# Optimization experiments

Hardware: AMD Instinct MI355X
Metric: run time of the kernel (lower is better)

The kernel has to match this reference:

```python
import jax, jax.numpy as jnp
import numpy as np

N_IN, N_OUT, H = 32, 31, 128
B1, B2 = 256, 256


def setup_inputs() -> dict:
    key = jax.random.key(0)
    ks = jax.random.split(key, 6)
    def lin(k, o, i):
        return jax.random.normal(k, (o, i), jnp.float32) / np.float32(np.sqrt(i))
    return {
        "t": jax.random.uniform(ks[0], (), jnp.float32),
        "y": jax.random.normal(ks[1], (B1, B2, N_OUT), jnp.float32),
        "W0": lin(ks[2], H, N_IN), "b0": jnp.zeros((H,), jnp.float32),
        "W1": lin(ks[3], H, H),    "b1": jnp.zeros((H,), jnp.float32),
        "W2": lin(ks[4], H, H),    "b2": jnp.zeros((H,), jnp.float32),
        "W3": lin(ks[5], N_OUT, H), "b3": jnp.zeros((N_OUT,), jnp.float32),
    }


def reference(t, y, W0, b0, W1, b1, W2, b2, W3, b3):
    # inp[..., :-1] = y ; inp[..., -1] = force(t) with force = sin
    force = jnp.sin(t)
    inp = jnp.concatenate(
        [y, jnp.broadcast_to(force, y.shape[:-1] + (1,))], axis=-1
    )  # [B1, B2, N_IN]

    def model(x):  # x: [N_IN]
        h = jnp.tanh(W0 @ x + b0)
        h = jnp.tanh(W1 @ h + b1)
        h = jnp.tanh(W2 @ h + b2)
        return W3 @ h + b3  # [N_OUT]

    out = jax.vmap(jax.vmap(model))(inp)  # [B1, B2, N_OUT]
    # vmap(vmap(jacrev(model)))(inp)[..., :-1] -> drop d/d(force) column
    jac = jax.vmap(jax.vmap(jax.jacrev(model)))(inp)[..., :-1]  # [B1,B2,N_OUT,N_IN-1]
    return out, jac
```

## Files before the change

kernel.cpp:

```cpp
#include <hip/hip_runtime.h>
#include <hip/hip_bf16.h>
#include <math.h>


using short8 = __attribute__((ext_vector_type(8))) short;
using f32x4  = __attribute__((ext_vector_type(4))) float;

#define WAVES 8
#define PB 4
#define PPB 32
#define STRIDE 136

__device__ __forceinline__ float fast_tanh(float z) {
    float e = __expf(2.0f * z);
    return 1.0f - 2.0f * __builtin_amdgcn_rcpf(e + 1.0f);
}

__device__ __forceinline__ ushort f2bf(float f) {
    union { float f; unsigned u; } v; v.f = f;
    unsigned r = v.u + 0x7fffu + ((v.u >> 16) & 1u);
    return (ushort)(r >> 16);
}

__device__ __forceinline__ short8 pack8(const float* s) {
    union { ushort u[8]; short8 v; } r;
    #pragma unroll
    for (int i = 0; i < 8; ++i) r.u[i] = f2bf(s[i]);
    return r.v;
}

__global__ void __launch_bounds__(512, 4)
node_mfma(const float* __restrict__ tptr,
          const float* __restrict__ y,
          const float* __restrict__ W0, const float* __restrict__ b0,
          const float* __restrict__ W1, const float* __restrict__ b1,
          const float* __restrict__ W2, const float* __restrict__ b2,
          const float* __restrict__ W3, const float* __restrict__ b3,
          float* __restrict__ out, float* __restrict__ jac, int npts) {
    __shared__ ushort XT[PB][32][STRIDE];
    __shared__ float  xb[PB][32];

    const int tid  = threadIdx.x;
    const int w    = tid >> 6;
    const int lane = tid & 63;
    const int r16  = lane & 15;
    const int g    = lane >> 4;
    const int j    = 16 * w + r16;

    float w0f[8];
    {
        const float4* p4 = reinterpret_cast<const float4*>(W0 + j * 32 + g * 8);
        float4 q0 = p4[0], q1 = p4[1];
        w0f[0]=q0.x; w0f[1]=q0.y; w0f[2]=q0.z; w0f[3]=q0.w;
        w0f[4]=q1.x; w0f[5]=q1.y; w0f[6]=q1.z; w0f[7]=q1.w;
    }
    short8 aW[2][4];
    #pragma unroll
    for (int L = 0; L < 2; ++L) {
        const float* WL = L ? W2 : W1;
        #pragma unroll
        for (int kc = 0; kc < 4; ++kc) {
            float tmp[8];
            const float4* p4 = reinterpret_cast<const float4*>(WL + j * 128 + kc * 32 + g * 8);
            float4 q0 = p4[0], q1 = p4[1];
            tmp[0]=q0.x; tmp[1]=q0.y; tmp[2]=q0.z; tmp[3]=q0.w;
            tmp[4]=q1.x; tmp[5]=q1.y; tmp[6]=q1.z; tmp[7]=q1.w;
            aW[L][kc] = pack8(tmp);
        }
    }
    const int mw = (w >> 1) & 1, nw = w & 1;
    const int r3 = 16 * mw + r16;
    short8 aW3[4];
    #pragma unroll
    for (int kc = 0; kc < 4; ++kc) {
        float tmp[8];
        if (r3 < 31) {
            const float4* p4 = reinterpret_cast<const float4*>(W3 + r3 * 128 + kc * 32 + g * 8);
            float4 q0 = p4[0], q1 = p4[1];
            tmp[0]=q0.x; tmp[1]=q0.y; tmp[2]=q0.z; tmp[3]=q0.w;
            tmp[4]=q1.x; tmp[5]=q1.y; tmp[6]=q1.z; tmp[7]=q1.w;
        } else {
            #pragma unroll
            for (int i = 0; i < 8; ++i) tmp[i] = 0.0f;
        }
        aW3[kc] = pack8(tmp);
    }
    const float b0v = b0[j];
    float bv[2][4], b3v[4];
    #pragma unroll
    for (int reg = 0; reg < 4; ++reg) {
        bv[0][reg] = b1[16 * w + 4 * g + reg];
        bv[1][reg] = b2[16 * w + 4 * g + reg];
        int o = 16 * mw + 4 * g + reg;
        b3v[reg] = (o < 31) ? b3[o] : 0.0f;
    }
    const float force = sinf(tptr[0]);

    for (int pass = 0; pass < PPB / PB; ++pass) {
        const int pbase = blockIdx.x * PPB + pass * PB;

        if (tid < PB * 32) {
            int pl = tid >> 5, c = tid & 31;
            float v = 0.0f;
            if (pbase + pl < npts) v = (c < 31) ? y[(size_t)(pbase + pl) * 31 + c] : force;
            xb[pl][c] = v;
        }
        __syncthreads();

        #pragma unroll
        for (int pl = 0; pl < PB; ++pl) {
            float zp = 0.0f;
            #pragma unroll
            for (int i = 0; i < 8; ++i) zp = fmaf(w0f[i], xb[pl][g * 8 + i], zp);
            zp += __shfl_xor(zp, 16, 64);
            zp += __shfl_xor(zp, 32, 64);
            float h = fast_tanh(zp + b0v);
            float d = 1.0f - h * h;
            #pragma unroll
            for (int i = 0; i < 8; ++i) {
                int c = g * 8 + i;
                XT[pl][c][j] = f2bf((c == 31) ? h : d * w0f[i]);
            }
        }
        __syncthreads();

        #pragma unroll
        for (int L = 0; L < 2; ++L) {
            uint2 stashA[PB], stashB[PB];
            #pragma unroll
            for (int pl = 0; pl < PB; ++pl) {
                f32x4 a0 = {0.f, 0.f, 0.f, 0.f}, a1 = {0.f, 0.f, 0.f, 0.f};
                #pragma unroll
                for (int kc = 0; kc < 4; ++kc) {
                    short8 bf0 = *reinterpret_cast<const short8*>(&XT[pl][r16][kc * 32 + g * 8]);
                    short8 bf1 = *reinterpret_cast<const short8*>(&XT[pl][16 + r16][kc * 32 + g * 8]);
                    a0 = __builtin_amdgcn_mfma_f32_16x16x32_bf16(aW[L][kc], bf0, a0, 0, 0, 0);
                    a1 = __builtin_amdgcn_mfma_f32_16x16x32_bf16(aW[L][kc], bf1, a1, 0, 0, 0);
                }
                union { ushort u[4]; uint2 v; } pa, pb;
                #pragma unroll
                for (int reg = 0; reg < 4; ++reg) {
                    float tv = fast_tanh(a1[reg] + bv[L][reg]);
                    float d  = 1.0f - tv * tv;
                    float dd = __shfl(d, lane | 15, 64);
                    pa.u[reg] = f2bf(dd * a0[reg]);
                    pb.u[reg] = (r16 == 15) ? f2bf(tv) : f2bf(dd * a1[reg]);
                }
                stashA[pl] = pa.v; stashB[pl] = pb.v;
            }
            __syncthreads();
            #pragma unroll
            for (int pl = 0; pl < PB; ++pl) {
                *reinterpret_cast<uint2*>(&XT[pl][r16][16 * w + 4 * g])      = stashA[pl];
                *reinterpret_cast<uint2*>(&XT[pl][16 + r16][16 * w + 4 * g]) = stashB[pl];
            }
            __syncthreads();
        }

        #pragma unroll
        for (int tsk = 0; tsk < 2; ++tsk) {
            int pl = (w >> 2) + tsk * 2;
            f32x4 a = {0.f, 0.f, 0.f, 0.f};
            #pragma unroll
            for (int kc = 0; kc < 4; ++kc) {
                short8 bf = *reinterpret_cast<const short8*>(&XT[pl][16 * nw + r16][kc * 32 + g * 8]);
                a = __builtin_amdgcn_mfma_f32_16x16x32_bf16(aW3[kc], bf, a, 0, 0, 0);
            }
            size_t p = (size_t)(pbase + pl);
            int c = 16 * nw + r16;
            if ((int)p < npts) {
                #pragma unroll
                for (int reg = 0; reg < 4; ++reg) {
                    int o = 16 * mw + 4 * g + reg;
                    if (o < 31) {
                        if (c == 31) out[p * 31 + o] = a[reg] + b3v[reg];
                        else         jac[(p * 31 + o) * 31 + c] = a[reg];
                    }
                }
            }
        }
        __syncthreads();
    }
}

extern "C" void kernel_launch(void* const* d_in, const int* in_sizes, int n_in,
                              void* d_out, int out_size, void* d_ws, size_t ws_size,
                              hipStream_t stream) {
    const float* t  = (const float*)d_in[0];
    const float* y  = (const float*)d_in[1];
    const float* W0 = (const float*)d_in[2];
    const float* b0 = (const float*)d_in[3];
    const float* W1 = (const float*)d_in[4];
    const float* b1 = (const float*)d_in[5];
    const float* W2 = (const float*)d_in[6];
    const float* b2 = (const float*)d_in[7];
    const float* W3 = (const float*)d_in[8];
    const float* b3 = (const float*)d_in[9];

    const int npts = in_sizes[1] / 31;
    float* out = (float*)d_out;
    float* jac = out + (size_t)npts * 31;

    const int blocks = (npts + PPB - 1) / PPB;
    node_mfma<<<blocks, 512, 0, stream>>>(t, y, W0, b0, W1, b1, W2, b2, W3, b3,
                                          out, jac, npts);
}
```

Baseline: 385.8 us.

## Stage Jacobian outputs in LDS for coalesced stores and use packed bf16 conversion

Jacobian and output tiles are first written into shared memory (reusing the XT buffer) and then stored to global memory with contiguous per-point writes. Before, each lane scattered strided stores straight from the MFMA accumulators. The layer-0 Jacobian seed is rebuilt from a bf16 transposed copy of W0 in LDS plus staged h/d vectors, and each thread writes packed 4-element chunks instead of 8 scalar bf16 stores. The f2bf bit trick is replaced by the hardware v_cvt_pk_bf16_f32 instruction. This adds extra barriers and LDS traffic, and the layer-0 seed now uses a bf16-rounded W0 rather than the fp32 W0.

Result: slower. 403.6 us (+4.6%).

```diff
diff --git a/kernel.cpp b/kernel.cpp
--- a/kernel.cpp
+++ b/kernel.cpp
@@ -6,7 +6,6 @@
 using short8 = __attribute__((ext_vector_type(8))) short;
 using f32x4  = __attribute__((ext_vector_type(4))) float;
 
-#define WAVES 8
 #define PB 4
 #define PPB 32
 #define STRIDE 136
@@ -16,16 +15,27 @@
     return 1.0f - 2.0f * __builtin_amdgcn_rcpf(e + 1.0f);
 }
 
-__device__ __forceinline__ ushort f2bf(float f) {
+__device__ __forceinline__ unsigned pk2(float lo, float hi) {
+    unsigned r;
+    asm("v_cvt_pk_bf16_f32 %0, %1, %2" : "=v"(r) : "v"(lo), "v"(hi));
+    return r;
+}
+
+__device__ __forceinline__ float bf2f(ushort u) {
+    union { unsigned u; float f; } c; c.u = ((unsigned)u) << 16;
+    return c.f;
+}
+
+__device__ __forceinline__ ushort f2bf1(float f) {
     union { float f; unsigned u; } v; v.f = f;
     unsigned r = v.u + 0x7fffu + ((v.u >> 16) & 1u);
     return (ushort)(r >> 16);
 }
 
-__device__ __forceinline__ short8 pack8(const float* s) {
-    union { ushort u[8]; short8 v; } r;
-    #pragma unroll
-    for (int i = 0; i < 8; ++i) r.u[i] = f2bf(s[i]);
+__device__ __forceinline__ short8 pack8f(const float* s) {
+    union { unsigned u[4]; short8 v; } r;
+    #pragma unroll
+    for (int q = 0; q < 4; ++q) r.u[q] = pk2(s[2 * q], s[2 * q + 1]);
     return r.v;
 }
 
@@ -37,8 +47,14 @@
           const float* __restrict__ W2, const float* __restrict__ b2,
           const float* __restrict__ W3, const float* __restrict__ b3,
           float* __restrict__ out, float* __restrict__ jac, int npts) {
-    __shared__ ushort XT[PB][32][STRIDE];
-    __shared__ float  xb[PB][32];
+    __shared__ __align__(16) ushort XT[PB][32][STRIDE];
+    __shared__ __align__(16) ushort W0T[32][128];
+    __shared__ __align__(16) float  d0s[PB][128];
+    __shared__ __align__(16) float  h0s[PB][128];
+    __shared__ float xb[PB][32];
+    __shared__ float ostage[PB][31];
+
+    float* jstage = reinterpret_cast<float*>(&XT[0][0][0]);
 
     const int tid  = threadIdx.x;
     const int w    = tid >> 6;
@@ -47,6 +63,11 @@
     const int g    = lane >> 4;
     const int j    = 16 * w + r16;
 
+    for (int e = tid; e < 4096; e += 512) {
+        int jj = e >> 5, c = e & 31;
+        W0T[c][jj] = f2bf1(W0[e]);
+    }
+
     float w0f[8];
     {
         const float4* p4 = reinterpret_cast<const float4*>(W0 + j * 32 + g * 8);
@@ -65,7 +86,7 @@
             float4 q0 = p4[0], q1 = p4[1];
             tmp[0]=q0.x; tmp[1]=q0.y; tmp[2]=q0.z; tmp[3]=q0.w;
             tmp[4]=q1.x; tmp[5]=q1.y; tmp[6]=q1.z; tmp[7]=q1.w;
-            aW[L][kc] = pack8(tmp);
+            aW[L][kc] = pack8f(tmp);
         }
     }
     const int mw = (w >> 1) & 1, nw = w & 1;
@@ -83,7 +104,7 @@
             #pragma unroll
             for (int i = 0; i < 8; ++i) tmp[i] = 0.0f;
         }
-        aW3[kc] = pack8(tmp);
+        aW3[kc] = pack8f(tmp);
     }
     const float b0v = b0[j];
     float bv[2][4], b3v[4];
@@ -115,12 +136,30 @@
             zp += __shfl_xor(zp, 16, 64);
             zp += __shfl_xor(zp, 32, 64);
             float h = fast_tanh(zp + b0v);
-            float d = 1.0f - h * h;
-            #pragma unroll
-            for (int i = 0; i < 8; ++i) {
-                int c = g * 8 + i;
-                XT[pl][c][j] = f2bf((c == 31) ? h : d * w0f[i]);
-            }
+            if (g == 0) {
+                h0s[pl][j] = h;
+                d0s[pl][j] = 1.0f - h * h;
+            }
+        }
+        __syncthreads();
+
+        #pragma unroll
+        for (int it = 0; it < 8; ++it) {
+            int idx = (it << 9) + tid;
+            int pl = idx >> 10, rem = idx & 1023;
+            int c = rem >> 5, jq = rem & 31;
+            float v0, v1, v2, v3;
+            if (c == 31) {
+                float4 hv = *reinterpret_cast<const float4*>(&h0s[pl][4 * jq]);
+                v0 = hv.x; v1 = hv.y; v2 = hv.z; v3 = hv.w;
+            } else {
+                float4 dv = *reinterpret_cast<const float4*>(&d0s[pl][4 * jq]);
+                ushort4 wv = *reinterpret_cast<const ushort4*>(&W0T[c][4 * jq]);
+                v0 = bf2f(wv.x) * dv.x; v1 = bf2f(wv.y) * dv.y;
+                v2 = bf2f(wv.z) * dv.z; v3 = bf2f(wv.w) * dv.w;
+            }
+            uint2 o; o.x = pk2(v0, v1); o.y = pk2(v2, v3);
+            *reinterpret_cast<uint2*>(&XT[pl][c][4 * jq]) = o;
         }
         __syncthreads();
 
@@ -137,16 +176,19 @@
                     a0 = __builtin_amdgcn_mfma_f32_16x16x32_bf16(aW[L][kc], bf0, a0, 0, 0, 0);
                     a1 = __builtin_amdgcn_mfma_f32_16x16x32_bf16(aW[L][kc], bf1, a1, 0, 0, 0);
                 }
-                union { ushort u[4]; uint2 v; } pa, pb;
+                float va[4], vb[4];
                 #pragma unroll
                 for (int reg = 0; reg < 4; ++reg) {
                     float tv = fast_tanh(a1[reg] + bv[L][reg]);
                     float d  = 1.0f - tv * tv;
                     float dd = __shfl(d, lane | 15, 64);
-                    pa.u[reg] = f2bf(dd * a0[reg]);
-                    pb.u[reg] = (r16 == 15) ? f2bf(tv) : f2bf(dd * a1[reg]);
+                    va[reg] = dd * a0[reg];
+                    vb[reg] = (r16 == 15) ? tv : dd * a1[reg];
                 }
-                stashA[pl] = pa.v; stashB[pl] = pb.v;
+                uint2 pa, pb;
+                pa.x = pk2(va[0], va[1]); pa.y = pk2(va[2], va[3]);
+                pb.x = pk2(vb[0], vb[1]); pb.y = pk2(vb[2], vb[3]);
+                stashA[pl] = pa; stashB[pl] = pb;
             }
             __syncthreads();
             #pragma unroll
@@ -157,6 +199,7 @@
             __syncthreads();
         }
 
+        f32x4 at[2];
         #pragma unroll
         for (int tsk = 0; tsk < 2; ++tsk) {
             int pl = (w >> 2) + tsk * 2;
@@ -166,18 +209,37 @@
                 short8 bf = *reinterpret_cast<const short8*>(&XT[pl][16 * nw + r16][kc * 32 + g * 8]);
                 a = __builtin_amdgcn_mfma_f32_16x16x32_bf16(aW3[kc], bf, a, 0, 0, 0);
             }
-            size_t p = (size_t)(pbase + pl);
+            at[tsk] = a;
+        }
+        __syncthreads();
+
+        #pragma unroll
+        for (int tsk = 0; tsk < 2; ++tsk) {
+            int pl = (w >> 2) + tsk * 2;
             int c = 16 * nw + r16;
+            #pragma unroll
+            for (int reg = 0; reg < 4; ++reg) {
+                int o = 16 * mw + 4 * g + reg;
+                if (o < 31) {
+                    if (c == 31)      ostage[pl][o] = at[tsk][reg] + b3v[reg];
+                    else              jstage[pl * 961 + o * 31 + c] = at[tsk][reg];
+                }
+            }
+        }
+        __syncthreads();
+
+        #pragma unroll
+        for (int pl = 0; pl < PB; ++pl) {
+            size_t p = (size_t)pbase + pl;
             if ((int)p < npts) {
-                #pragma unroll
-                for (int reg = 0; reg < 4; ++reg) {
-                    int o = 16 * mw + 4 * g + reg;
-                    if (o < 31) {
-                        if (c == 31) out[p * 31 + o] = a[reg] + b3v[reg];
-                        else         jac[(p * 31 + o) * 31 + c] = a[reg];
-                    }
-                }
-            }
+                for (int e = tid; e < 961; e += 512)
+                    jac[p * 961 + e] = jstage[pl * 961 + e];
+            }
+        }
+        if (tid < 128) {
+            int pl = tid >> 5, o = tid & 31;
+            if (o < 31 && pbase + pl < npts)
+                out[(size_t)(pbase + pl) * 31 + o] = ostage[pl][o];
         }
         __syncthreads();
     }
```

## Double-buffer activations in LDS, prefetch next y, use packed bf16 convert

Applied to the files above, without the earlier changes.

Splits the shared activation tile into two buffers so each hidden layer writes its output into the other buffer. This removes one barrier per layer and the register stash, and the barrier at the end of each pass is also dropped. The next pass's input row is prefetched from global memory into a register while the current pass computes. Float-to-bf16 rounding now uses the hardware v_cvt_pk_bf16_f32 instruction, and s_setprio is raised around the MFMA loops. The cost is twice the LDS footprint, which could reduce occupancy, and the prefetch drops the npts bounds check, so a partial last block would read past the end of y.

Result: faster. 322.4 us (-16.4%).

```diff
diff --git a/kernel.cpp b/kernel.cpp
--- a/kernel.cpp
+++ b/kernel.cpp
@@ -6,7 +6,6 @@
 using short8 = __attribute__((ext_vector_type(8))) short;
 using f32x4  = __attribute__((ext_vector_type(4))) float;
 
-#define WAVES 8
 #define PB 4
 #define PPB 32
 #define STRIDE 136
@@ -16,16 +15,22 @@
     return 1.0f - 2.0f * __builtin_amdgcn_rcpf(e + 1.0f);
 }
 
-__device__ __forceinline__ ushort f2bf(float f) {
+__device__ __forceinline__ unsigned pk2(float lo, float hi) {
+    unsigned r;
+    asm("v_cvt_pk_bf16_f32 %0, %1, %2" : "=v"(r) : "v"(lo), "v"(hi));
+    return r;
+}
+
+__device__ __forceinline__ ushort f2bf1(float f) {
     union { float f; unsigned u; } v; v.f = f;
     unsigned r = v.u + 0x7fffu + ((v.u >> 16) & 1u);
     return (ushort)(r >> 16);
 }
 
-__device__ __forceinline__ short8 pack8(const float* s) {
-    union { ushort u[8]; short8 v; } r;
-    #pragma unroll
-    for (int i = 0; i < 8; ++i) r.u[i] = f2bf(s[i]);
+__device__ __forceinline__ short8 pack8f(const float* s) {
+    union { unsigned u[4]; short8 v; } r;
+    #pragma unroll
+    for (int q = 0; q < 4; ++q) r.u[q] = pk2(s[2 * q], s[2 * q + 1]);
     return r.v;
 }
 
@@ -37,8 +42,8 @@
           const float* __restrict__ W2, const float* __restrict__ b2,
           const float* __restrict__ W3, const float* __restrict__ b3,
           float* __restrict__ out, float* __restrict__ jac, int npts) {
-    __shared__ ushort XT[PB][32][STRIDE];
-    __shared__ float  xb[PB][32];
+    __shared__ __align__(16) ushort XT[2][PB][32][STRIDE];
+    __shared__ float xb[PB][32];
 
     const int tid  = threadIdx.x;
     const int w    = tid >> 6;
@@ -65,7 +70,7 @@
             float4 q0 = p4[0], q1 = p4[1];
             tmp[0]=q0.x; tmp[1]=q0.y; tmp[2]=q0.z; tmp[3]=q0.w;
             tmp[4]=q1.x; tmp[5]=q1.y; tmp[6]=q1.z; tmp[7]=q1.w;
-            aW[L][kc] = pack8(tmp);
+            aW[L][kc] = pack8f(tmp);
         }
     }
     const int mw = (w >> 1) & 1, nw = w & 1;
@@ -83,7 +88,7 @@
             #pragma unroll
             for (int i = 0; i < 8; ++i) tmp[i] = 0.0f;
         }
-        aW3[kc] = pack8(tmp);
+        aW3[kc] = pack8f(tmp);
     }
     const float b0v = b0[j];
     float bv[2][4], b3v[4];
@@ -96,15 +101,15 @@
     }
     const float force = sinf(tptr[0]);
 
+    const int pl0 = tid >> 5, c0 = tid & 31;
+    const bool act = tid < PB * 32;
+    float pf = 0.0f;
+    if (act && c0 < 31) pf = y[(size_t)(blockIdx.x * PPB + pl0) * 31 + c0];
+
     for (int pass = 0; pass < PPB / PB; ++pass) {
         const int pbase = blockIdx.x * PPB + pass * PB;
 
-        if (tid < PB * 32) {
-            int pl = tid >> 5, c = tid & 31;
-            float v = 0.0f;
-            if (pbase + pl < npts) v = (c < 31) ? y[(size_t)(pbase + pl) * 31 + c] : force;
-            xb[pl][c] = v;
-        }
+        if (act) xb[pl0][c0] = (c0 < 31) ? pf : force;
         __syncthreads();
 
         #pragma unroll
@@ -119,40 +124,43 @@
             #pragma unroll
             for (int i = 0; i < 8; ++i) {
                 int c = g * 8 + i;
-                XT[pl][c][j] = f2bf((c == 31) ? h : d * w0f[i]);
-            }
-        }
+                XT[0][pl][c][j] = f2bf1((c == 31) ? h : d * w0f[i]);
+            }
+        }
+
+        if (act && c0 < 31 && pass + 1 < PPB / PB)
+            pf = y[(size_t)(pbase + PB + pl0) * 31 + c0];
+
         __syncthreads();
 
         #pragma unroll
         for (int L = 0; L < 2; ++L) {
-            uint2 stashA[PB], stashB[PB];
             #pragma unroll
             for (int pl = 0; pl < PB; ++pl) {
                 f32x4 a0 = {0.f, 0.f, 0.f, 0.f}, a1 = {0.f, 0.f, 0.f, 0.f};
+                __builtin_amdgcn_s_setprio(1);
                 #pragma unroll
                 for (int kc = 0; kc < 4; ++kc) {
-                    short8 bf0 = *reinterpret_cast<const short8*>(&XT[pl][r16][kc * 32 + g * 8]);
-                    short8 bf1 = *reinterpret_cast<const short8*>(&XT[pl][16 + r16][kc * 32 + g * 8]);
+                    short8 bf0 = *reinterpret_cast<const short8*>(&XT[L][pl][r16][kc * 32 + g * 8]);
+                    short8 bf1 = *reinterpret_cast<const short8*>(&XT[L][pl][16 + r16][kc * 32 + g * 8]);
                     a0 = __builtin_amdgcn_mfma_f32_16x16x32_bf16(aW[L][kc], bf0, a0, 0, 0, 0);
                     a1 = __builtin_amdgcn_mfma_f32_16x16x32_bf16(aW[L][kc], bf1, a1, 0, 0, 0);
                 }
-                union { ushort u[4]; uint2 v; } pa, pb;
+                __builtin_amdgcn_s_setprio(0);
+                float va[4], vb[4];
                 #pragma unroll
                 for (int reg = 0; reg < 4; ++reg) {
                     float tv = fast_tanh(a1[reg] + bv[L][reg]);
                     float d  = 1.0f - tv * tv;
                     float dd = __shfl(d, lane | 15, 64);
-                    pa.u[reg] = f2bf(dd * a0[reg]);
-                    pb.u[reg] = (r16 == 15) ? f2bf(tv) : f2bf(dd * a1[reg]);
+                    va[reg] = dd * a0[reg];
+                    vb[reg] = (r16 == 15) ? tv : dd * a1[reg];
                 }
-                stashA[pl] = pa.v; stashB[pl] = pb.v;
-            }
-            __syncthreads();
-            #pragma unroll
-            for (int pl = 0; pl < PB; ++pl) {
-                *reinterpret_cast<uint2*>(&XT[pl][r16][16 * w + 4 * g])      = stashA[pl];
-                *reinterpret_cast<uint2*>(&XT[pl][16 + r16][16 * w + 4 * g]) = stashB[pl];
+                uint2 pa, pb;
+                pa.x = pk2(va[0], va[1]); pa.y = pk2(va[2], va[3]);
+                pb.x = pk2(vb[0], vb[1]); pb.y = pk2(vb[2], vb[3]);
+                *reinterpret_cast<uint2*>(&XT[1 - L][pl][r16][16 * w + 4 * g])      = pa;
+                *reinterpret_cast<uint2*>(&XT[1 - L][pl][16 + r16][16 * w + 4 * g]) = pb;
             }
             __syncthreads();
         }
@@ -161,11 +169,13 @@
         for (int tsk = 0; tsk < 2; ++tsk) {
             int pl = (w >> 2) + tsk * 2;
             f32x4 a = {0.f, 0.f, 0.f, 0.f};
+            __builtin_amdgcn_s_setprio(1);
             #pragma unroll
             for (int kc = 0; kc < 4; ++kc) {
-                short8 bf = *reinterpret_cast<const short8*>(&XT[pl][16 * nw + r16][kc * 32 + g * 8]);
+                short8 bf = *reinterpret_cast<const short8*>(&XT[0][pl][16 * nw + r16][kc * 32 + g * 8]);
                 a = __builtin_amdgcn_mfma_f32_16x16x32_bf16(aW3[kc], bf, a, 0, 0, 0);
             }
+            __builtin_amdgcn_s_setprio(0);
             size_t p = (size_t)(pbase + pl);
             int c = 16 * nw + r16;
             if ((int)p < npts) {
@@ -179,7 +189,6 @@
                 }
             }
         }
-        __syncthreads();
     }
 }
 
```
